# Kernel tuning notes

Hardware: AMD Instinct MI355X
Metric: run time of the kernel (lower is better)

Reference implementation:

```python
import jax, jax.numpy as jnp
import numpy as np
from jax import lax

T, B, NPG, F_IN = 10, 8, 1080, 2
N = B * NPG            # 8640 nodes total
DEG = 16
E = N * DEG            # 138240 edges
HID, HEADS = 64, 8
LSTM_H, OUT = 128, 2
NEG_SLOPE = 0.2

# (in_dim, heads, out_channels_per_head) for the 4 GATConv layers
LAYER_DIMS = [(F_IN, HEADS, HID), (HID * HEADS, HEADS, HID // 2),
              (HID // 2 * HEADS, HEADS, HID // 4), (HID // 4 * HEADS, 1, HID // 8)]


def setup_inputs() -> dict:
    key = jax.random.key(0)
    ks = iter(jax.random.split(key, 40))
    inp = {}
    inp['x_seq'] = jax.random.normal(next(ks), (T, N, F_IN), jnp.float32)
    # kNN-style edges within each graph: every node receives DEG random in-graph neighbors
    dst = jnp.repeat(jnp.arange(N, dtype=jnp.int32), DEG)
    offs = (dst // NPG) * NPG
    src = offs + jax.random.randint(next(ks), (E,), 0, NPG, jnp.int32)
    inp['edge_index'] = jnp.stack([src, dst])
    inp['batch'] = jnp.repeat(jnp.arange(B, dtype=jnp.int32), NPG)
    # GAT params: W [in, H*C], att_src/att_dst [H, C], bias [H*C]
    for li, (fin, h, c) in enumerate(LAYER_DIMS, start=1):
        s = 1.0 / np.sqrt(fin)
        inp[f'W{li}'] = jax.random.uniform(next(ks), (fin, h * c), jnp.float32, -s, s)
        inp[f'as{li}'] = jax.random.uniform(next(ks), (h, c), jnp.float32, -s, s)
        inp[f'ad{li}'] = jax.random.uniform(next(ks), (h, c), jnp.float32, -s, s)
        inp[f'b{li}'] = jnp.zeros((h * c,), jnp.float32)
    # LSTM (PyTorch layout, gate order i,f,g,o)
    gdim = HID // 8
    sl = 1.0 / np.sqrt(LSTM_H)
    inp['w_ih'] = jax.random.uniform(next(ks), (4 * LSTM_H, gdim), jnp.float32, -sl, sl)
    inp['w_hh'] = jax.random.uniform(next(ks), (4 * LSTM_H, LSTM_H), jnp.float32, -sl, sl)
    inp['b_ih'] = jax.random.uniform(next(ks), (4 * LSTM_H,), jnp.float32, -sl, sl)
    inp['b_hh'] = jax.random.uniform(next(ks), (4 * LSTM_H,), jnp.float32, -sl, sl)
    inp['w_fc'] = jax.random.uniform(next(ks), (OUT, LSTM_H), jnp.float32, -sl, sl)
    inp['b_fc'] = jax.random.uniform(next(ks), (OUT,), jnp.float32, -sl, sl)
    return inp


def _forward(x_seq, W1, as1, ad1, b1, W2, as2, ad2, b2, W3, as3, ad3, b3,
             W4, as4, ad4, b4, w_ih, w_hh, b_ih, b_hh, w_fc, b_fc,
             edge_index, batch):
    # PyG GATConv adds self-loops by default
    loops = jnp.arange(N, dtype=edge_index.dtype)
    src = jnp.concatenate([edge_index[0], loops])
    dst = jnp.concatenate([edge_index[1], loops])

    def gat(x, W, a_s, a_d, b):
        Hh, C = a_s.shape
        h = (x @ W).reshape(N, Hh, C)                 # [N,H,C]
        e_s = (h * a_s).sum(-1)                        # [N,H]
        e_d = (h * a_d).sum(-1)
        e = jax.nn.leaky_relu(e_s[src] + e_d[dst], NEG_SLOPE)   # [Etot,H]
        m = jax.ops.segment_max(e, dst, num_segments=N)
        ex = jnp.exp(e - m[dst])
        den = jax.ops.segment_sum(ex, dst, num_segments=N)
        alpha = ex / (den[dst] + 1e-16)
        out = jax.ops.segment_sum(h[src] * alpha[:, :, None], dst, num_segments=N)
        return out.reshape(N, Hh * C) + b

    counts = jax.ops.segment_sum(jnp.ones((N,), jnp.float32), batch, num_segments=B)[:, None]

    def per_t(x):  # eval mode: dropout = identity
        x = jax.nn.elu(gat(x, W1, as1, ad1, b1))
        x = jax.nn.elu(gat(x, W2, as2, ad2, b2))
        x = jax.nn.elu(gat(x, W3, as3, ad3, b3))
        x = jax.nn.elu(gat(x, W4, as4, ad4, b4))
        return jax.ops.segment_sum(x, batch, num_segments=B) / counts  # mean pool [B, hid//8]

    _, embs = lax.scan(lambda c, xt: (c, per_t(xt)), None, x_seq)  # [T,B,gdim]

    h0 = jnp.zeros((B, LSTM_H), x_seq.dtype)
    c0 = jnp.zeros((B, LSTM_H), x_seq.dtype)

    def step(carry, xt):
        h, c = carry
        g = xt @ w_ih.T + h @ w_hh.T + b_ih + b_hh
        i, f, gg, o = jnp.split(g, 4, axis=-1)
        c = jax.nn.sigmoid(f) * c + jax.nn.sigmoid(i) * jnp.tanh(gg)
        h = jax.nn.sigmoid(o) * jnp.tanh(c)
        return (h, c), None

    (h_last, _), _ = lax.scan(step, (h0, c0), embs)
    return h_last @ w_fc.T + b_fc  # [B, OUT] (eval path: last timestep only)


def reference(x_seq, W1, as1, ad1, b1, W2, as2, ad2, b2, W3, as3, ad3, b3,
              W4, as4, ad4, b4, w_ih, w_hh, b_ih, b_hh, w_fc, b_fc,
              edge_index, batch):
    return _forward(x_seq, W1, as1, ad1, b1, W2, as2, ad2, b2, W3, as3, ad3, b3,
                    W4, as4, ad4, b4, w_ih, w_hh, b_ih, b_hh, w_fc, b_fc,
                    edge_index, batch)
```

## Files before the change

### kernel.cpp

```cpp
#include <hip/hip_runtime.h>
#include <math.h>

#define T_TOT 10
#define NB    8
#define NPG   1080
#define NN    (NB*NPG)
#define DEG   16

typedef unsigned short ushortT;
using short8 = __attribute__((ext_vector_type(8))) short;
using f32x4  = __attribute__((ext_vector_type(4))) float;

__device__ __forceinline__ float lrelu(float v) { return v > 0.f ? v : 0.2f*v; }
__device__ __forceinline__ float elu1(float v)  { return v > 0.f ? v : (__expf(v) - 1.f); }
__device__ __forceinline__ float bf2f(ushortT h){ return __uint_as_float(((unsigned)h) << 16); }
__device__ __forceinline__ float bfl(unsigned u){ return __uint_as_float(u << 16); }
__device__ __forceinline__ float bfh(unsigned u){ return __uint_as_float(u & 0xFFFF0000u); }
__device__ __forceinline__ ushortT rne(float v) {
    unsigned u = __float_as_uint(v);
    u += 0x7FFFu + ((u >> 16) & 1u);
    return (ushortT)(u >> 16);
}
__device__ __forceinline__ unsigned pk2(float a, float b) {
    return (unsigned)rne(a) | ((unsigned)rne(b) << 16);
}
__device__ __forceinline__ int xswz(int b, int nwg) {
    int q = nwg >> 3, r = nwg & 7;
    int x = b & 7, i = b >> 3;
    return x*q + min(x, r) + i;
}

__global__ void k_prep_l1(const float* __restrict__ W1, const float* __restrict__ as1,
                          const float* __restrict__ ad1, float* __restrict__ A) {
    int tid = threadIdx.x;
    if (tid >= 32) return;
    int h = tid & 7, k = (tid >> 3) & 1, sd = tid >> 4;
    const float* att = sd ? ad1 : as1;
    float acc = 0.f;
    for (int c = 0; c < 64; ++c) acc += W1[k*512 + h*64 + c] * att[h*64 + c];
    A[sd*16 + k*8 + h] = acc;
}

__global__ void k_prepW(const float* __restrict__ W, ushortT* __restrict__ WT, int K, int M) {
    int i = blockIdx.x*256 + threadIdx.x;
    if (i >= K*M) return;
    int k = i / M, m = i - k*M;
    WT[(size_t)m*K + k] = rne(W[i]);
}

__global__ __launch_bounds__(256) void k_gat1(
    const float* __restrict__ x, const int* __restrict__ esrc,
    const float* __restrict__ A, const float* __restrict__ W1,
    const float* __restrict__ b1, ushortT* __restrict__ q, int R) {
    int tid = threadIdx.x;
    int g = xswz(blockIdx.x, gridDim.x)*32 + (tid >> 3);
    int l = tid & 7;
    if (g >= R*8) g = R*8 - 1;
    int r = g >> 3, hh = g & 7;
    int t = r / NN, n = r - t*NN;
    float2 xr = *(const float2*)&x[2*r];
    float As0 = A[hh], As1 = A[8+hh];
    float edv = xr.x*A[16+hh] + xr.y*A[24+hh];
    float ev[3], xs0[3], xs1[3];
    float m = -1e30f;
    #pragma unroll
    for (int s = 0; s < 3; ++s) {
        int j = s*8 + l;
        if (j < 17) {
            int src = (j == 16) ? r : (t*NN + esrc[n*DEG + j]);
            float2 xs = *(const float2*)&x[2*src];
            xs0[s] = xs.x; xs1[s] = xs.y;
            float e = lrelu(xs.x*As0 + xs.y*As1 + edv);
            ev[s] = e; m = fmaxf(m, e);
        } else { ev[s] = -1e30f; xs0[s] = 0.f; xs1[s] = 0.f; }
    }
    #pragma unroll
    for (int off = 4; off >= 1; off >>= 1) m = fmaxf(m, __shfl_xor(m, off, 8));
    float den = 0.f, p0 = 0.f, p1 = 0.f;
    #pragma unroll
    for (int s = 0; s < 3; ++s) {
        float e2 = __expf(ev[s] - m);
        den += e2; p0 += e2*xs0[s]; p1 += e2*xs1[s];
    }
    #pragma unroll
    for (int off = 4; off >= 1; off >>= 1) {
        den += __shfl_xor(den, off, 8);
        p0  += __shfl_xor(p0,  off, 8);
        p1  += __shfl_xor(p1,  off, 8);
    }
    float inv = 1.f/(den + 1e-16f);
    float xa0 = p0*inv, xa1 = p1*inv;
    int col = hh*64 + l*8;
    float4 w0a = *(const float4*)&W1[col],       w0b = *(const float4*)&W1[col+4];
    float4 w1a = *(const float4*)&W1[512+col],   w1b = *(const float4*)&W1[512+col+4];
    float4 bba = *(const float4*)&b1[col],       bbb = *(const float4*)&b1[col+4];
    float v0 = elu1(xa0*w0a.x + xa1*w1a.x + bba.x);
    float v1 = elu1(xa0*w0a.y + xa1*w1a.y + bba.y);
    float v2 = elu1(xa0*w0a.z + xa1*w1a.z + bba.z);
    float v3 = elu1(xa0*w0a.w + xa1*w1a.w + bba.w);
    float v4 = elu1(xa0*w0b.x + xa1*w1b.x + bbb.x);
    float v5 = elu1(xa0*w0b.y + xa1*w1b.y + bbb.y);
    float v6 = elu1(xa0*w0b.z + xa1*w1b.z + bbb.z);
    float v7 = elu1(xa0*w0b.w + xa1*w1b.w + bbb.w);
    uint4 o;
    o.x = pk2(v0,v1); o.y = pk2(v2,v3); o.z = pk2(v4,v5); o.w = pk2(v6,v7);
    *(uint4*)&q[(size_t)r*512 + col] = o;
}

template<int H, int C, int LANES, bool BFIN, bool BFOUT>
__global__ __launch_bounds__(256) void k_gat(
    const void* __restrict__ hb_, const int* __restrict__ esrc,
    const float* __restrict__ es, const float* __restrict__ ed,
    const float* __restrict__ bias, float* __restrict__ out,
    ushortT* __restrict__ ohi, int R) {
    constexpr int CPL = C/LANES;
    constexpr int GPB = 256/LANES;
    constexpr int EPL = (17 + LANES - 1)/LANES;
    constexpr int HC = H*C;
    int tid = threadIdx.x;
    int l = tid & (LANES-1);
    int g = xswz(blockIdx.x, gridDim.x)*GPB + tid/LANES;
    if (g >= R*H) g = R*H - 1;
    int r = g / H, hh = g % H;
    int t = r / NN, n = r - t*NN;
    float edv = ed[(size_t)r*H + hh];
    float ev[EPL]; int sv[EPL];
    float m = -1e30f;
    #pragma unroll
    for (int s = 0; s < EPL; ++s) {
        int j = s*LANES + l;
        if (j < 17) {
            int src = (j == 16) ? r : (t*NN + esrc[n*DEG + j]);
            sv[s] = src;
            float e = lrelu(es[(size_t)src*H + hh] + edv);
            ev[s] = e; m = fmaxf(m, e);
        } else { ev[s] = -1e30f; sv[s] = r; }
    }
    #pragma unroll
    for (int off = LANES/2; off >= 1; off >>= 1) m = fmaxf(m, __shfl_xor(m, off, LANES));
    float den = 0.f;
    float wv[EPL];
    #pragma unroll
    for (int s = 0; s < EPL; ++s) {
        float e2 = __expf(ev[s] - m);
        wv[s] = e2; den += e2;
    }
    #pragma unroll
    for (int off = LANES/2; off >= 1; off >>= 1) den += __shfl_xor(den, off, LANES);
    float inv = 1.f/(den + 1e-16f);
    #pragma unroll
    for (int s = 0; s < EPL; ++s) wv[s] *= inv;

    int lb = (tid & 63) & ~(LANES-1);
    float acc[CPL] = {};
    #pragma unroll
    for (int j = 0; j < 17; ++j) {
        float wj = __shfl(wv[j/LANES], lb + (j & (LANES-1)), 64);
        int   sj = __shfl(sv[j/LANES], lb + (j & (LANES-1)), 64);
        if constexpr (BFIN) {
            const ushortT* hp = (const ushortT*)hb_ + (size_t)sj*HC + hh*C + l*CPL;
            uint4 hv = *(const uint4*)hp;
            acc[0] += wj*bfl(hv.x); acc[1] += wj*bfh(hv.x);
            acc[2] += wj*bfl(hv.y); acc[3] += wj*bfh(hv.y);
            acc[4] += wj*bfl(hv.z); acc[5] += wj*bfh(hv.z);
            acc[6] += wj*bfl(hv.w); acc[7] += wj*bfh(hv.w);
        } else {
            const float* hp = (const float*)hb_ + (size_t)sj*HC + hh*C + l*CPL;
            float4 hv = *(const float4*)hp;
            acc[0] += wj*hv.x; acc[1] += wj*hv.y;
            acc[2] += wj*hv.z; acc[3] += wj*hv.w;
        }
    }
    int base = hh*C + l*CPL;
    #pragma unroll
    for (int c = 0; c < CPL; ++c) acc[c] = elu1(acc[c] + bias[base + c]);
    if constexpr (BFOUT) {
        uint4 o;
        o.x = pk2(acc[0],acc[1]); o.y = pk2(acc[2],acc[3]);
        o.z = pk2(acc[4],acc[5]); o.w = pk2(acc[6],acc[7]);
        *(uint4*)&ohi[(size_t)r*HC + base] = o;
    } else {
        *(float4*)&out[(size_t)r*HC + base] = make_float4(acc[0],acc[1],acc[2],acc[3]);
    }
}

template<int C>
__global__ __launch_bounds__(256) void k_gemm_mfma(
    const ushortT* __restrict__ X, const ushortT* __restrict__ WT,
    const float* __restrict__ as_, const float* __restrict__ ad_,
    ushortT* __restrict__ Hout, float* __restrict__ es, float* __restrict__ ed,
    int R, int K, int M) {
    __shared__ __align__(16) char smem[32768];
    int tid = threadIdx.x;
    int wid = tid >> 6, l = tid & 63;
    int l15 = l & 15, lg = l >> 4;
    int wr = wid >> 1, wc = wid & 1;
    int rb = blockIdx.x*128, cb = blockIdx.y*128;

    f32x4 acc[4][4] = {};
    int aoff[4], asw[4], boff[4], bsw[4];
    #pragma unroll
    for (int i = 0; i < 4; ++i) {
        int ar = wr*64 + i*16 + l15;
        aoff[i] = ar*128; asw[i] = (ar & 7) << 4;
        int bc = wc*64 + i*16 + l15;
        boff[i] = 16384 + bc*128; bsw[i] = (bc & 7) << 4;
    }
    int kb0 = lg*16;
    const size_t strideB = (size_t)K*2;
    int srow = tid >> 3, sc8 = tid & 7;
    int ssw = ((srow & 7) << 4);
    const int nKT = K >> 6;

    for (int kt = 0; kt < nKT; ++kt) {
        int kbyte = kt*128;
        __syncthreads();
        #pragma unroll
        for (int i = 0; i < 4; ++i) {
            int row = srow + i*32;
            int dst = row*128 + ((sc8*16) ^ ssw);
            int rg = min(rb + row, R - 1);
            uint4 va = *(const uint4*)((const char*)X  + (size_t)rg*strideB + kbyte + sc8*16);
            uint4 vw = *(const uint4*)((const char*)WT + (size_t)(cb + row)*strideB + kbyte + sc8*16);
            *(uint4*)(smem + dst)         = va;
            *(uint4*)(smem + 16384 + dst) = vw;
        }
        __syncthreads();
        #pragma unroll
        for (int ks = 0; ks < 2; ++ks) {
            int kb = ks*64 + kb0;
            short8 ah[4], bv[4];
            #pragma unroll
            for (int i = 0; i < 4; ++i) {
                ah[i] = *(const short8*)(smem + aoff[i] + (kb ^ asw[i]));
                bv[i] = *(const short8*)(smem + boff[i] + (kb ^ bsw[i]));
            }
            #pragma unroll
            for (int mt = 0; mt < 4; ++mt)
                #pragma unroll
                for (int nt = 0; nt < 4; ++nt)
                    acc[mt][nt] = __builtin_amdgcn_mfma_f32_16x16x32_bf16(ah[mt], bv[nt], acc[mt][nt], 0, 0, 0);
        }
    }
    __syncthreads();
    constexpr int NSL = 128/C;
    constexpr int NHW = 64/C;
    int hg0 = cb / C;
    float asv[4], adv[4];
    #pragma unroll
    for (int nt = 0; nt < 4; ++nt) {
        int col = wc*64 + nt*16 + l15;
        int h = col / C, c = col - h*C;
        asv[nt] = as_[(hg0 + h)*C + c];
        adv[nt] = ad_[(hg0 + h)*C + c];
    }
    float* ebp = (float*)smem;
    #pragma unroll
    for (int mt = 0; mt < 4; ++mt) {
        float ps[4][NHW] = {}, pd[4][NHW] = {};
        #pragma unroll
        for (int nt = 0; nt < 4; ++nt) {
            int sl = (nt*16)/C;
            #pragma unroll
            for (int q = 0; q < 4; ++q) {
                ps[q][sl] += acc[mt][nt][q]*asv[nt];
                pd[q][sl] += acc[mt][nt][q]*adv[nt];
            }
        }
        #pragma unroll
        for (int off = 1; off < 16; off <<= 1)
            #pragma unroll
            for (int q = 0; q < 4; ++q)
                #pragma unroll
                for (int sl = 0; sl < NHW; ++sl) {
                    ps[q][sl] += __shfl_xor(ps[q][sl], off);
                    pd[q][sl] += __shfl_xor(pd[q][sl], off);
                }
        if (l15 == 0) {
            #pragma unroll
            for (int q = 0; q < 4; ++q) {
                int row = wr*64 + mt*16 + lg*4 + q;
                #pragma unroll
                for (int sl = 0; sl < NHW; ++sl) {
                    ebp[(row*NSL + wc*NHW + sl)*2 + 0] = ps[q][sl];
                    ebp[(row*NSL + wc*NHW + sl)*2 + 1] = pd[q][sl];
                }
            }
        }
        #pragma unroll
        for (int nt = 0; nt < 4; ++nt) {
            int col = cb + wc*64 + nt*16 + l15;
            #pragma unroll
            for (int q = 0; q < 4; ++q) {
                int r = rb + wr*64 + mt*16 + lg*4 + q;
                if (r < R) Hout[(size_t)r*M + col] = rne(acc[mt][nt][q]);
            }
        }
    }
    __syncthreads();
    for (int i = tid; i < 128*NSL; i += 256) {
        int row = i / NSL, sl = i - row*NSL;
        int r = rb + row;
        if (r < R) {
            es[(size_t)r*8 + hg0 + sl] = ebp[i*2 + 0];
            ed[(size_t)r*8 + hg0 + sl] = ebp[i*2 + 1];
        }
    }
}

__global__ __launch_bounds__(256) void k_lin4(
    const ushortT* __restrict__ X, const float* __restrict__ W,
    const float* __restrict__ as_, const float* __restrict__ ad_,
    float* __restrict__ Hout, float* __restrict__ es, float* __restrict__ ed, int R) {
    int tid = threadIdx.x;
    int l = tid & 7;
    int r = blockIdx.x*32 + (tid >> 3);
    if (r >= R) return;
    const ushortT* xp = X + (size_t)r*128 + l*16;
    uint4 a = *(const uint4*)xp;
    uint4 b = *(const uint4*)(xp + 8);
    float xv[16];
    xv[0]=bfl(a.x); xv[1]=bfh(a.x); xv[2]=bfl(a.y); xv[3]=bfh(a.y);
    xv[4]=bfl(a.z); xv[5]=bfh(a.z); xv[6]=bfl(a.w); xv[7]=bfh(a.w);
    xv[8]=bfl(b.x); xv[9]=bfh(b.x); xv[10]=bfl(b.y); xv[11]=bfh(b.y);
    xv[12]=bfl(b.z); xv[13]=bfh(b.z); xv[14]=bfl(b.w); xv[15]=bfh(b.w);
    float acc[8] = {};
    #pragma unroll
    for (int kk = 0; kk < 16; ++kk) {
        const float* wr = W + (l*16 + kk)*8;
        float4 wa = *(const float4*)wr, wb = *(const float4*)(wr + 4);
        acc[0] += xv[kk]*wa.x; acc[1] += xv[kk]*wa.y;
        acc[2] += xv[kk]*wa.z; acc[3] += xv[kk]*wa.w;
        acc[4] += xv[kk]*wb.x; acc[5] += xv[kk]*wb.y;
        acc[6] += xv[kk]*wb.z; acc[7] += xv[kk]*wb.w;
    }
    #pragma unroll
    for (int off = 4; off >= 1; off >>= 1)
        #pragma unroll
        for (int c = 0; c < 8; ++c) acc[c] += __shfl_xor(acc[c], off, 8);
    if (l == 0) {
        *(float4*)&Hout[(size_t)r*8]     = make_float4(acc[0],acc[1],acc[2],acc[3]);
        *(float4*)&Hout[(size_t)r*8 + 4] = make_float4(acc[4],acc[5],acc[6],acc[7]);
        float ps = 0.f, pd = 0.f;
        #pragma unroll
        for (int c = 0; c < 8; ++c) { ps += acc[c]*as_[c]; pd += acc[c]*ad_[c]; }
        es[r] = ps; ed[r] = pd;
    }
}

__global__ void k_pool(const float* __restrict__ x4, float* __restrict__ emb, int t0) {
    __shared__ float red[256];
    int tl = blockIdx.x >> 3, b = blockIdx.x & 7;
    int tid = threadIdx.x;
    int c = tid & 7, nl = tid >> 3;
    float s = 0.f;
    for (int k = 0; k < 34; ++k) {
        int n = nl + 32*k;
        if (n < NPG) s += x4[((size_t)tl*NN + b*NPG + n)*8 + c];
    }
    red[tid] = s;
    __syncthreads();
    for (int st = 16; st >= 1; st >>= 1) {
        if (nl < st) red[tid] += red[tid + st*8];
        __syncthreads();
    }
    if (nl == 0) emb[((t0 + tl)*8 + b)*8 + c] = red[c] * (1.f/1080.f);
}

__global__ __launch_bounds__(512) void k_lstm(
    const float* __restrict__ emb, const float* __restrict__ w_ih,
    const float* __restrict__ w_hh, const float* __restrict__ b_ih,
    const float* __restrict__ b_hh, const float* __restrict__ w_fc,
    const float* __restrict__ b_fc, float* __restrict__ out) {
    int b = blockIdx.x, u = threadIdx.x;
    __shared__ float h[128], cst[128], g[512], eall[T_TOT*8];
    if (u < 128) { h[u] = 0.f; cst[u] = 0.f; }
    if (u < T_TOT*8) eall[u] = emb[((u >> 3)*8 + b)*8 + (u & 7)];
    float wreg[128];
    {
        const float* wp = w_hh + (size_t)u*128;
        #pragma unroll
        for (int k4 = 0; k4 < 32; ++k4) {
            float4 v = *(const float4*)&wp[k4*4];
            wreg[4*k4+0] = v.x; wreg[4*k4+1] = v.y;
            wreg[4*k4+2] = v.z; wreg[4*k4+3] = v.w;
        }
    }
    float wih[8];
    #pragma unroll
    for (int k = 0; k < 8; ++k) wih[k] = w_ih[(size_t)u*8 + k];
    float bsum = b_ih[u] + b_hh[u];
    __syncthreads();
    for (int t = 0; t < T_TOT; ++t) {
        float a0 = bsum, a1 = 0.f, a2 = 0.f, a3 = 0.f;
        #pragma unroll
        for (int k = 0; k < 8; ++k) a0 += eall[t*8 + k]*wih[k];
        #pragma unroll
        for (int k = 0; k < 32; ++k) {
            a0 += h[4*k+0]*wreg[4*k+0];
            a1 += h[4*k+1]*wreg[4*k+1];
            a2 += h[4*k+2]*wreg[4*k+2];
            a3 += h[4*k+3]*wreg[4*k+3];
        }
        g[u] = (a0 + a1) + (a2 + a3);
        __syncthreads();
        if (u < 128) {
            float ig = 1.f/(1.f + __expf(-g[u]));
            float fg = 1.f/(1.f + __expf(-g[128+u]));
            float gg = tanhf(g[256+u]);
            float og = 1.f/(1.f + __expf(-g[384+u]));
            float cn = fg*cst[u] + ig*gg;
            cst[u] = cn;
            h[u] = og*tanhf(cn);
        }
        __syncthreads();
    }
    if (u < 64) {
        float p0 = h[u]*w_fc[u]       + h[u+64]*w_fc[64+u];
        float p1 = h[u]*w_fc[128+u]   + h[u+64]*w_fc[192+u];
        #pragma unroll
        for (int off = 32; off >= 1; off >>= 1) {
            p0 += __shfl_xor(p0, off, 64);
            p1 += __shfl_xor(p1, off, 64);
        }
        if (u == 0) {
            out[b*2 + 0] = p0 + b_fc[0];
            out[b*2 + 1] = p1 + b_fc[1];
        }
    }
}

extern "C" void kernel_launch(void* const* d_in, const int* in_sizes, int n_in,
                              void* d_out, int out_size, void* d_ws, size_t ws_size,
                              hipStream_t stream) {
    const float* x_seq = (const float*)d_in[0];
    const int*   edge  = (const int*)d_in[1];
    const float* W1 = (const float*)d_in[3];
    const float* as1 = (const float*)d_in[4];
    const float* ad1 = (const float*)d_in[5];
    const float* b1  = (const float*)d_in[6];
    const float* W2 = (const float*)d_in[7];
    const float* as2 = (const float*)d_in[8];
    const float* ad2 = (const float*)d_in[9];
    const float* b2  = (const float*)d_in[10];
    const float* W3 = (const float*)d_in[11];
    const float* as3 = (const float*)d_in[12];
    const float* ad3 = (const float*)d_in[13];
    const float* b3  = (const float*)d_in[14];
    const float* W4 = (const float*)d_in[15];
    const float* as4 = (const float*)d_in[16];
    const float* ad4 = (const float*)d_in[17];
    const float* b4  = (const float*)d_in[18];
    const float* w_ih = (const float*)d_in[19];
    const float* w_hh = (const float*)d_in[20];
    const float* b_ih = (const float*)d_in[21];
    const float* b_hh = (const float*)d_in[22];
    const float* w_fc = (const float*)d_in[23];
    const float* b_fc = (const float*)d_in[24];

    char* w = (char*)d_ws;
    auto alloc = [&](size_t bytes) {
        char* p = w; w += (bytes + 255) & ~(size_t)255; return p;
    };
    float*   A1  = (float*)alloc(128);
    float*   emb = (float*)alloc((size_t)T_TOT*8*8*4);
    ushortT* W2T = (ushortT*)alloc((size_t)256*512*2);
    ushortT* W3T = (ushortT*)alloc((size_t)128*256*2);
    size_t used = (size_t)(w - (char*)d_ws);
    size_t perT = (size_t)NN*(1024 + 512 + 512 + 256 + 256 + 128);
    size_t rem = (ws_size > used + 4096) ? ws_size - used - 4096 : 0;
    int Tc = (int)(rem / perT);
    if (Tc > T_TOT) Tc = T_TOT;
    if (Tc < 1) Tc = 1;
    ushortT* Q  = (ushortT*)alloc((size_t)Tc*NN*1024);
    ushortT* P  = (ushortT*)alloc((size_t)Tc*NN*512);
    ushortT* G3 = (ushortT*)alloc((size_t)Tc*NN*512);
    ushortT* H3 = (ushortT*)alloc((size_t)Tc*NN*256);
    ushortT* G4 = (ushortT*)alloc((size_t)Tc*NN*256);
    float*   ES = (float*)alloc((size_t)Tc*NN*32);
    float*   ED = (float*)alloc((size_t)Tc*NN*32);
    float*   P4 = (float*)alloc((size_t)Tc*NN*32);
    float*   G5 = (float*)alloc((size_t)Tc*NN*32);

    k_prep_l1<<<1, 64, 0, stream>>>(W1, as1, ad1, A1);
    k_prepW<<<(256*512 + 255)/256, 256, 0, stream>>>(W2, W2T, 512, 256);
    k_prepW<<<(128*256 + 255)/256, 256, 0, stream>>>(W3, W3T, 256, 128);

    for (int t0 = 0; t0 < T_TOT; t0 += Tc) {
        int tc = (Tc < T_TOT - t0) ? Tc : (T_TOT - t0);
        int R = tc*NN;
        int nrb = (R + 127)/128;
        const float* xoff = x_seq + (size_t)t0*NN*2;
        k_gat1<<<(R*8 + 31)/32, 256, 0, stream>>>(xoff, edge, A1, W1, b1, Q, R);
        k_gemm_mfma<32><<<dim3(nrb, 2), 256, 0, stream>>>(Q, W2T, as2, ad2, P, ES, ED, R, 512, 256);
        k_gat<8,32,4,true,true><<<(R*8 + 63)/64, 256, 0, stream>>>(P, edge, ES, ED, b2, nullptr, G3, R);
        k_gemm_mfma<16><<<dim3(nrb, 1), 256, 0, stream>>>(G3, W3T, as3, ad3, H3, ES, ED, R, 256, 128);
        k_gat<8,16,2,true,true><<<(R*8 + 127)/128, 256, 0, stream>>>(H3, edge, ES, ED, b3, nullptr, G4, R);
        k_lin4<<<(R + 31)/32, 256, 0, stream>>>(G4, W4, as4, ad4, P4, ES, ED, R);
        k_gat<1,8,2,false,false><<<(R + 127)/128, 256, 0, stream>>>(P4, edge, ES, ED, b4, G5, nullptr, R);
        k_pool<<<tc*8, 256, 0, stream>>>(G5, emb, t0);
    }
    k_lstm<<<8, 512, 0, stream>>>(emb, w_ih, w_hh, b_ih, b_hh, w_fc, b_fc, (float*)d_out);
}
```

Baseline: 400.6 us.

## Double-buffer MFMA GEMM tiles with direct global-to-LDS loads

The GEMM main loop now uses two LDS buffers, prefetching the next K tile while MFMAs consume the current one. Staging uses global_load_lds so data goes straight into LDS without passing through registers, and the XOR swizzle moves to the source address. The goal is to hide global load latency and drop a sync per iteration, at the cost of doubling LDS to 64KB, which can reduce occupancy. With global_load_lds and only a trailing barrier, correctness depends on the compiler inserting the right vmcnt waits before the barrier.

Result: no change. 397.1 us (-0.9%).

```diff
diff --git a/kernel.cpp b/kernel.cpp
--- a/kernel.cpp
+++ b/kernel.cpp
@@ -28,6 +28,16 @@
     int q = nwg >> 3, r = nwg & 7;
     int x = b & 7, i = b >> 3;
     return x*q + min(x, r) + i;
+}
+__device__ __forceinline__ void gld16(const void* g, void* lbase, int laneoff) {
+#if __has_builtin(__builtin_amdgcn_global_load_lds)
+    typedef __attribute__((address_space(1))) const unsigned int GU;
+    typedef __attribute__((address_space(3))) unsigned int LU;
+    __builtin_amdgcn_global_load_lds((GU*)g, (LU*)lbase, 16, 0, 0);
+    (void)laneoff;
+#else
+    *(uint4*)((char*)lbase + laneoff) = *(const uint4*)g;
+#endif
 }
 
 __global__ void k_prep_l1(const float* __restrict__ W1, const float* __restrict__ as1,
@@ -190,12 +200,14 @@
     const float* __restrict__ as_, const float* __restrict__ ad_,
     ushortT* __restrict__ Hout, float* __restrict__ es, float* __restrict__ ed,
     int R, int K, int M) {
-    __shared__ __align__(16) char smem[32768];
+    __shared__ __align__(16) char smem[65536];
     int tid = threadIdx.x;
     int wid = tid >> 6, l = tid & 63;
     int l15 = l & 15, lg = l >> 4;
     int wr = wid >> 1, wc = wid & 1;
     int rb = blockIdx.x*128, cb = blockIdx.y*128;
+    const size_t strideB = (size_t)K*2;
+    const int nKT = K >> 6;
 
     f32x4 acc[4][4] = {};
     int aoff[4], asw[4], boff[4], bsw[4];
@@ -207,33 +219,38 @@
         boff[i] = 16384 + bc*128; bsw[i] = (bc & 7) << 4;
     }
     int kb0 = lg*16;
-    const size_t strideB = (size_t)K*2;
-    int srow = tid >> 3, sc8 = tid & 7;
-    int ssw = ((srow & 7) << 4);
-    const int nKT = K >> 6;
-
+    int srowL = wid*8 + (l >> 3);
+    int scolb = (l & 7)*16;
+
+    auto stage = [&](int buf, int kt) {
+        int kbyte = kt*128;
+        char* base = smem + (buf << 15);
+        #pragma unroll
+        for (int i = 0; i < 4; ++i) {
+            int row = i*32 + srowL;
+            int colb = scolb ^ ((row & 7) << 4);
+            const char* sa = (const char*)X  + (size_t)min(rb + row, R - 1)*strideB + kbyte + colb;
+            const char* sb = (const char*)WT + (size_t)(cb + row)*strideB + kbyte + colb;
+            int dchunk = (i*32 + wid*8)*128;
+            gld16(sa, base + dchunk,         l*16);
+            gld16(sb, base + 16384 + dchunk, l*16);
+        }
+    };
+
+    stage(0, 0);
+    __syncthreads();
     for (int kt = 0; kt < nKT; ++kt) {
-        int kbyte = kt*128;
-        __syncthreads();
-        #pragma unroll
-        for (int i = 0; i < 4; ++i) {
-            int row = srow + i*32;
-            int dst = row*128 + ((sc8*16) ^ ssw);
-            int rg = min(rb + row, R - 1);
-            uint4 va = *(const uint4*)((const char*)X  + (size_t)rg*strideB + kbyte + sc8*16);
-            uint4 vw = *(const uint4*)((const char*)WT + (size_t)(cb + row)*strideB + kbyte + sc8*16);
-            *(uint4*)(smem + dst)         = va;
-            *(uint4*)(smem + 16384 + dst) = vw;
-        }
-        __syncthreads();
+        int cur = kt & 1;
+        if (kt + 1 < nKT) stage(cur ^ 1, kt + 1);
+        const char* bufp = smem + (cur << 15);
         #pragma unroll
         for (int ks = 0; ks < 2; ++ks) {
             int kb = ks*64 + kb0;
             short8 ah[4], bv[4];
             #pragma unroll
             for (int i = 0; i < 4; ++i) {
-                ah[i] = *(const short8*)(smem + aoff[i] + (kb ^ asw[i]));
-                bv[i] = *(const short8*)(smem + boff[i] + (kb ^ bsw[i]));
+                ah[i] = *(const short8*)(bufp + aoff[i] + (kb ^ asw[i]));
+                bv[i] = *(const short8*)(bufp + boff[i] + (kb ^ bsw[i]));
             }
             #pragma unroll
             for (int mt = 0; mt < 4; ++mt)
@@ -241,8 +258,8 @@
                 for (int nt = 0; nt < 4; ++nt)
                     acc[mt][nt] = __builtin_amdgcn_mfma_f32_16x16x32_bf16(ah[mt], bv[nt], acc[mt][nt], 0, 0, 0);
         }
-    }
-    __syncthreads();
+        __syncthreads();
+    }
     constexpr int NSL = 128/C;
     constexpr int NHW = 64/C;
     int hg0 = cb / C;
```
